# Optimization experiments

Measured on AMD Instinct MI355X. Metric: run time of the kernel, lower is better.

The kernel has to match this reference:

```python
import jax, jax.numpy as jnp
import numpy as np

N_USERS = 100000
N_ITEMS = 50000
N = N_USERS + N_ITEMS
EMBED_DIM = 64
N_LAYERS = 3
NNZ = 4800000


def setup_inputs() -> dict:
    key = jax.random.key(0)
    k1, k2, k3, k4, k5 = jax.random.split(key, 5)
    user_emb = jax.random.normal(k1, (N_USERS, EMBED_DIM), dtype=jnp.float32)
    item_emb = jax.random.normal(k2, (N_ITEMS, EMBED_DIM), dtype=jnp.float32)
    adj_row = jax.random.randint(k3, (NNZ,), 0, N, dtype=jnp.int32)
    adj_col = jax.random.randint(k4, (NNZ,), 0, N, dtype=jnp.int32)
    # normalized adjacency values (positive, small) like D^-1/2 A D^-1/2
    adj_vals = jax.random.uniform(k5, (NNZ,), dtype=jnp.float32) * 0.05
    return {"user_emb": user_emb, "item_emb": item_emb,
            "adj_row": adj_row, "adj_col": adj_col, "adj_vals": adj_vals}


def _spmm(vals, row, col, x):
    # sparse (N,N) @ dense (N,d) via gather + segment_sum
    return jax.ops.segment_sum(vals[:, None] * x[col], row, num_segments=N)


def reference(user_emb, item_emb, adj_row, adj_col, adj_vals):
    all_emb = jnp.concatenate([user_emb, item_emb], axis=0)  # (N, d)
    acc = all_emb  # running sum of layer outputs (fused mean)
    cur = all_emb
    for _ in range(N_LAYERS):
        cur = _spmm(adj_vals, adj_row, adj_col, cur)
        acc = acc + cur
    final_emb = acc / jnp.float32(N_LAYERS + 1)
    return final_emb[:N_USERS], final_emb[N_USERS:]
```

## Files before the change

kernel.cpp:

```cpp
#include <hip/hip_runtime.h>

#define N_USERS 100000
#define N_ITEMS 50000
#define N_TOTAL 150000
#define DIM 64
#define NNZ_C 4800000
#define NELEM (N_TOTAL * DIM)
#define NELEM4 (NELEM / 4)

#define RPB 74
#define NB 2048
#define NBLK 512
#define CHUNK (NNZ_C / NBLK)
#define CAP 4096

typedef unsigned short ush;

__device__ __forceinline__ float bf2f(ush u) {
    return __uint_as_float(((unsigned)u) << 16);
}
__device__ __forceinline__ ush f2bf(float f) {
    unsigned u = __float_as_uint(f);
    return (ush)((u + 0x7fffu + ((u >> 16) & 1u)) >> 16);
}

__global__ __launch_bounds__(256) void init_kernel(
    const float4* __restrict__ user, const float4* __restrict__ item,
    ushort4* __restrict__ A16) {
    int i = blockIdx.x * 256 + threadIdx.x;
    if (i >= NELEM4) return;
    const int u4 = N_USERS * DIM / 4;
    float4 v = (i < u4) ? user[i] : item[i - u4];
    ushort4 b;
    b.x = f2bf(v.x); b.y = f2bf(v.y); b.z = f2bf(v.z); b.w = f2bf(v.w);
    A16[i] = b;
}

__global__ __launch_bounds__(1024) void p1_hist(
    const int* __restrict__ row, int* __restrict__ histmat) {
    __shared__ int h[NB];
    int t = threadIdx.x, b = blockIdx.x;
    for (int j = t; j < NB; j += 1024) h[j] = 0;
    __syncthreads();
    int kbeg = b * CHUNK, kend = kbeg + CHUNK;
    for (int k = kbeg + t; k < kend; k += 1024) {
        unsigned r = (unsigned)row[k];
        atomicAdd(&h[r / RPB], 1);
    }
    __syncthreads();
    for (int j = t; j < NB; j += 1024) histmat[b * NB + j] = h[j];
}

__global__ __launch_bounds__(256) void p2a_colscan(
    const int* __restrict__ histmat, int* __restrict__ basemat,
    int* __restrict__ T) {
    int j = blockIdx.x * 256 + threadIdx.x;
    int run = 0;
    for (int b = 0; b < NBLK; b++) {
        basemat[b * NB + j] = run;
        run += histmat[b * NB + j];
    }
    T[j] = run;
}

__global__ __launch_bounds__(1024) void p2b_scan(
    const int* __restrict__ T, int* __restrict__ bucketbase,
    int* __restrict__ rowptr) {
    __shared__ int s[1024];
    int t = threadIdx.x;
    int v0 = T[2 * t], v1 = T[2 * t + 1];
    int pair = v0 + v1;
    s[t] = pair;
    __syncthreads();
    for (int off = 1; off < 1024; off <<= 1) {
        int w = (t >= off) ? s[t - off] : 0;
        __syncthreads();
        s[t] += w;
        __syncthreads();
    }
    int excl = s[t] - pair;
    bucketbase[2 * t] = excl;
    bucketbase[2 * t + 1] = excl + v0;
    if (t == 1023) { bucketbase[NB] = s[t]; rowptr[N_TOTAL] = NNZ_C; }
}

__global__ __launch_bounds__(1024) void p3_scatter(
    const int* __restrict__ row, const int* __restrict__ col,
    const float* __restrict__ vals, const int* __restrict__ histmat,
    const int* __restrict__ basemat, const int* __restrict__ bucketbase,
    uint2* __restrict__ entries) {
    __shared__ int s[1024];
    __shared__ int wp[NB];
    __shared__ int gbase[NB];
    __shared__ uint2 sorted[CHUNK];
    __shared__ int dest[CHUNK];
    int t = threadIdx.x, b = blockIdx.x;

    int c0 = histmat[b * NB + 2 * t];
    int c1 = histmat[b * NB + 2 * t + 1];
    int pair = c0 + c1;
    s[t] = pair;
    __syncthreads();
    for (int off = 1; off < 1024; off <<= 1) {
        int w = (t >= off) ? s[t - off] : 0;
        __syncthreads();
        s[t] += w;
        __syncthreads();
    }
    int excl = s[t] - pair;
    wp[2 * t] = excl;
    wp[2 * t + 1] = excl + c0;
    gbase[2 * t]     = bucketbase[2 * t]     + basemat[b * NB + 2 * t]     - excl;
    gbase[2 * t + 1] = bucketbase[2 * t + 1] + basemat[b * NB + 2 * t + 1] - (excl + c0);
    __syncthreads();

    int kbeg = b * CHUNK, kend = kbeg + CHUNK;
    for (int k = kbeg + t; k < kend; k += 1024) {
        unsigned r = (unsigned)row[k];
        unsigned j = r / RPB;
        unsigned rl = r - j * RPB;
        int pos = atomicAdd(&wp[j], 1);
        sorted[pos] = make_uint2((rl << 18) | (unsigned)col[k],
                                 __float_as_uint(vals[k]));
        dest[pos] = gbase[j] + pos;
    }
    __syncthreads();
    for (int i = t; i < CHUNK; i += 1024)
        entries[dest[i]] = sorted[i];
}

__global__ __launch_bounds__(512) void p4_sort(
    const int* __restrict__ bucketbase, uint2* __restrict__ entries,
    int* __restrict__ rowptr) {
    __shared__ uint2 stage[CAP];
    __shared__ int cnt[128], scanb[128], wp[128];
    int t = threadIdx.x, b = blockIdx.x;
    int base = bucketbase[b];
    int n = bucketbase[b + 1] - base;
    if (n > CAP) n = CAP;
    if (t < 128) cnt[t] = 0;
    __syncthreads();
    for (int i = t; i < n; i += 512) {
        uint2 e = entries[base + i];
        stage[i] = e;
        atomicAdd(&cnt[e.x >> 18], 1);
    }
    __syncthreads();
    if (t < 128) scanb[t] = cnt[t];
    __syncthreads();
    for (int off = 1; off < 128; off <<= 1) {
        int w = 0;
        if (t < 128 && t >= off) w = scanb[t - off];
        __syncthreads();
        if (t < 128) scanb[t] += w;
        __syncthreads();
    }
    if (t < RPB) {
        int excl = scanb[t] - cnt[t];
        wp[t] = excl;
        int rg = b * RPB + t;
        if (rg < N_TOTAL) rowptr[rg] = base + excl;
    }
    __syncthreads();
    for (int i = t; i < n; i += 512) {
        uint2 e = stage[i];
        unsigned rl = e.x >> 18;
        int pos = atomicAdd(&wp[rl], 1);
        ((int2*)entries)[base + pos] =
            make_int2((int)(e.x & 0x3FFFFu), (int)e.y);
    }
}

__global__ __launch_bounds__(256) void spmm_csr_kernel(
    const int* __restrict__ rowptr, const int2* __restrict__ csr,
    const ushort4* __restrict__ x4, ushort4* __restrict__ y4) {
    int gid = blockIdx.x * 256 + threadIdx.x;
    int lane = threadIdx.x & 63;
    int group = lane >> 4;
    int chunk = lane & 15;
    int r = (gid >> 6) * 4 + group;
    if (r >= N_TOTAL) return;
    int start = rowptr[r], end = rowptr[r + 1];
    float4 acc = make_float4(0.f, 0.f, 0.f, 0.f);
    for (int j0 = start; j0 < end; j0 += 16) {
        int j = j0 + chunk;
        int2 pair = make_int2(0, 0);
        if (j < end) pair = csr[j];
        int cnt = min(16, end - j0);
        #pragma unroll 4
        for (int t = 0; t < cnt; t++) {
            int src = group * 16 + t;
            int cc = __shfl(pair.x, src);
            float vv = __int_as_float(__shfl(pair.y, src));
            ushort4 xv = x4[cc * 16 + chunk];
            acc.x += vv * bf2f(xv.x);
            acc.y += vv * bf2f(xv.y);
            acc.z += vv * bf2f(xv.z);
            acc.w += vv * bf2f(xv.w);
        }
    }
    int o = r * 16 + chunk;
    ushort4 yb;
    yb.x = f2bf(acc.x); yb.y = f2bf(acc.y);
    yb.z = f2bf(acc.z); yb.w = f2bf(acc.w);
    y4[o] = yb;
}

__global__ __launch_bounds__(256) void spmm_merge_kernel(
    const int* __restrict__ rowptr, const int2* __restrict__ csr,
    const ushort4* __restrict__ x4 , const ushort4* __restrict__ e0,
    const ushort4* __restrict__ e1, float4* __restrict__ out) {
    int gid = blockIdx.x * 256 + threadIdx.x;
    int lane = threadIdx.x & 63;
    int group = lane >> 4;
    int chunk = lane & 15;
    int r = (gid >> 6) * 4 + group;
    if (r >= N_TOTAL) return;
    int start = rowptr[r], end = rowptr[r + 1];
    float4 acc = make_float4(0.f, 0.f, 0.f, 0.f);
    for (int j0 = start; j0 < end; j0 += 16) {
        int j = j0 + chunk;
        int2 pair = make_int2(0, 0);
        if (j < end) pair = csr[j];
        int cnt = min(16, end - j0);
        #pragma unroll 4
        for (int t = 0; t < cnt; t++) {
            int src = group * 16 + t;
            int cc = __shfl(pair.x, src);
            float vv = __int_as_float(__shfl(pair.y, src));
            ushort4 xv = x4[cc * 16 + chunk];
            acc.x += vv * bf2f(xv.x);
            acc.y += vv * bf2f(xv.y);
            acc.z += vv * bf2f(xv.z);
            acc.w += vv * bf2f(xv.w);
        }
    }
    int o = r * 16 + chunk;
    ushort4 a = e0[o], b = e1[o], c = x4[o];
    float4 oo;
    oo.x = (bf2f(a.x) + bf2f(b.x) + bf2f(c.x) + acc.x) * 0.25f;
    oo.y = (bf2f(a.y) + bf2f(b.y) + bf2f(c.y) + acc.y) * 0.25f;
    oo.z = (bf2f(a.z) + bf2f(b.z) + bf2f(c.z) + acc.z) * 0.25f;
    oo.w = (bf2f(a.w) + bf2f(b.w) + bf2f(c.w) + acc.w) * 0.25f;
    out[o] = oo;
}

extern "C" void kernel_launch(void* const* d_in, const int* in_sizes, int n_in,
                              void* d_out, int out_size, void* d_ws, size_t ws_size,
                              hipStream_t stream) {
    const float* user_emb = (const float*)d_in[0];
    const float* item_emb = (const float*)d_in[1];
    const int*   adj_row  = (const int*)d_in[2];
    const int*   adj_col  = (const int*)d_in[3];
    const float* adj_vals = (const float*)d_in[4];
    float* out = (float*)d_out;

    ush*   A          = (ush*)d_ws;
    ush*   B          = A + NELEM;
    ush*   C          = B + NELEM;
    uint2* entries    = (uint2*)(C + NELEM);
    int*   histmat    = (int*)(entries + NNZ_C);
    int*   basemat    = histmat + NBLK * NB;
    int*   T          = basemat + NBLK * NB;
    int*   bucketbase = T + NB;
    int*   rowptr     = bucketbase + NB + 1;

    const int eltBlocks  = (NELEM4 + 255) / 256;
    const int spmmBlocks = N_TOTAL / 16;

    init_kernel<<<eltBlocks, 256, 0, stream>>>(
        (const float4*)user_emb, (const float4*)item_emb, (ushort4*)A);
    p1_hist<<<NBLK, 1024, 0, stream>>>(adj_row, histmat);
    p2a_colscan<<<NB / 256, 256, 0, stream>>>(histmat, basemat, T);
    p2b_scan<<<1, 1024, 0, stream>>>(T, bucketbase, rowptr);
    p3_scatter<<<NBLK, 1024, 0, stream>>>(adj_row, adj_col, adj_vals,
                                          histmat, basemat, bucketbase, entries);
    p4_sort<<<NB, 512, 0, stream>>>(bucketbase, entries, rowptr);

    spmm_csr_kernel<<<spmmBlocks, 256, 0, stream>>>(rowptr, (const int2*)entries,
        (const ushort4*)A, (ushort4*)B);
    spmm_csr_kernel<<<spmmBlocks, 256, 0, stream>>>(rowptr, (const int2*)entries,
        (const ushort4*)B, (ushort4*)C);
    spmm_merge_kernel<<<spmmBlocks, 256, 0, stream>>>(rowptr, (const int2*)entries,
        (const ushort4*)C, (const ushort4*)A, (const ushort4*)B, (float4*)out);
}
```

Baseline: 539.5 us.

## Replace column-scan kernel with atomic bucket totals and atomic cursor allocation

Removes the p2a_colscan kernel, a serial walk over 512 blocks that produced a per-block base matrix. Bucket totals are now accumulated with global atomics in the histogram kernel, and each scatter block reserves its slice of a bucket with an atomicAdd on a padded cursor array. This drops one launch and the base-matrix traffic. The cost is a memset, global atomic contention on padded counters, and block order within a bucket that is no longer deterministic, which p4_sort must tolerate.

```diff
diff --git a/kernel.cpp b/kernel.cpp
--- a/kernel.cpp
+++ b/kernel.cpp
@@ -13,6 +13,7 @@
 #define NBLK 512
 #define CHUNK (NNZ_C / NBLK)
 #define CAP 4096
+#define CPAD 16
 
 typedef unsigned short ush;
 
@@ -37,7 +38,8 @@
 }
 
 __global__ __launch_bounds__(1024) void p1_hist(
-    const int* __restrict__ row, int* __restrict__ histmat) {
+    const int* __restrict__ row, int* __restrict__ histmat,
+    int* __restrict__ T) {
     __shared__ int h[NB];
     int t = threadIdx.x, b = blockIdx.x;
     for (int j = t; j < NB; j += 1024) h[j] = 0;
@@ -48,27 +50,19 @@
         atomicAdd(&h[r / RPB], 1);
     }
     __syncthreads();
-    for (int j = t; j < NB; j += 1024) histmat[b * NB + j] = h[j];
-}
-
-__global__ __launch_bounds__(256) void p2a_colscan(
-    const int* __restrict__ histmat, int* __restrict__ basemat,
-    int* __restrict__ T) {
-    int j = blockIdx.x * 256 + threadIdx.x;
-    int run = 0;
-    for (int b = 0; b < NBLK; b++) {
-        basemat[b * NB + j] = run;
-        run += histmat[b * NB + j];
-    }
-    T[j] = run;
+    for (int j = t; j < NB; j += 1024) {
+        int c = h[j];
+        histmat[b * NB + j] = c;
+        if (c) atomicAdd(&T[j * CPAD], c);
+    }
 }
 
 __global__ __launch_bounds__(1024) void p2b_scan(
     const int* __restrict__ T, int* __restrict__ bucketbase,
-    int* __restrict__ rowptr) {
+    int* __restrict__ cursor, int* __restrict__ rowptr) {
     __shared__ int s[1024];
     int t = threadIdx.x;
-    int v0 = T[2 * t], v1 = T[2 * t + 1];
+    int v0 = T[(2 * t) * CPAD], v1 = T[(2 * t + 1) * CPAD];
     int pair = v0 + v1;
     s[t] = pair;
     __syncthreads();
@@ -81,14 +75,15 @@
     int excl = s[t] - pair;
     bucketbase[2 * t] = excl;
     bucketbase[2 * t + 1] = excl + v0;
+    cursor[(2 * t) * CPAD] = excl;
+    cursor[(2 * t + 1) * CPAD] = excl + v0;
     if (t == 1023) { bucketbase[NB] = s[t]; rowptr[N_TOTAL] = NNZ_C; }
 }
 
 __global__ __launch_bounds__(1024) void p3_scatter(
     const int* __restrict__ row, const int* __restrict__ col,
     const float* __restrict__ vals, const int* __restrict__ histmat,
-    const int* __restrict__ basemat, const int* __restrict__ bucketbase,
-    uint2* __restrict__ entries) {
+    int* __restrict__ cursor, uint2* __restrict__ entries) {
     __shared__ int s[1024];
     __shared__ int wp[NB];
     __shared__ int gbase[NB];
@@ -110,8 +105,10 @@
     int excl = s[t] - pair;
     wp[2 * t] = excl;
     wp[2 * t + 1] = excl + c0;
-    gbase[2 * t]     = bucketbase[2 * t]     + basemat[b * NB + 2 * t]     - excl;
-    gbase[2 * t + 1] = bucketbase[2 * t + 1] + basemat[b * NB + 2 * t + 1] - (excl + c0);
+    int g0 = c0 ? atomicAdd(&cursor[(2 * t) * CPAD], c0) : 0;
+    int g1 = c1 ? atomicAdd(&cursor[(2 * t + 1) * CPAD], c1) : 0;
+    gbase[2 * t]     = g0 - excl;
+    gbase[2 * t + 1] = g1 - (excl + c0);
     __syncthreads();
 
     int kbeg = b * CHUNK, kend = kbeg + CHUNK;
@@ -260,21 +257,22 @@
     ush*   C          = B + NELEM;
     uint2* entries    = (uint2*)(C + NELEM);
     int*   histmat    = (int*)(entries + NNZ_C);
-    int*   basemat    = histmat + NBLK * NB;
-    int*   T          = basemat + NBLK * NB;
-    int*   bucketbase = T + NB;
+    int*   T          = histmat + NBLK * NB;
+    int*   cursor     = T + NB * CPAD;
+    int*   bucketbase = cursor + NB * CPAD;
     int*   rowptr     = bucketbase + NB + 1;
 
     const int eltBlocks  = (NELEM4 + 255) / 256;
     const int spmmBlocks = N_TOTAL / 16;
 
+    hipMemsetAsync(T, 0, NB * CPAD * sizeof(int), stream);
+
     init_kernel<<<eltBlocks, 256, 0, stream>>>(
         (const float4*)user_emb, (const float4*)item_emb, (ushort4*)A);
-    p1_hist<<<NBLK, 1024, 0, stream>>>(adj_row, histmat);
-    p2a_colscan<<<NB / 256, 256, 0, stream>>>(histmat, basemat, T);
-    p2b_scan<<<1, 1024, 0, stream>>>(T, bucketbase, rowptr);
+    p1_hist<<<NBLK, 1024, 0, stream>>>(adj_row, histmat, T);
+    p2b_scan<<<1, 1024, 0, stream>>>(T, bucketbase, cursor, rowptr);
     p3_scatter<<<NBLK, 1024, 0, stream>>>(adj_row, adj_col, adj_vals,
-                                          histmat, basemat, bucketbase, entries);
+                                          histmat, cursor, entries);
     p4_sort<<<NB, 512, 0, stream>>>(bucketbase, entries, rowptr);
 
     spmm_csr_kernel<<<spmmBlocks, 256, 0, stream>>>(rowptr, (const int2*)entries,
```

New measurement: 600.1 us. 11.2% more time.

## Parallelize column scan of block histograms with tiled three-pass scan

Applied to the files above, without the earlier changes.

Replaces the serial per-column exclusive scan over 512 block histograms, which ran on only 8 blocks of 256 threads, with a three-pass tiled scan: per-tile sums, a scan over 32 tile sums, then per-tile expansion. The aim is to spread the sequential dependency chain across many more blocks and shorten the latency of this phase. The cost is two extra kernel launches and an extra read of the histogram matrix plus small tile buffers in workspace.

```diff
diff --git a/kernel.cpp b/kernel.cpp
--- a/kernel.cpp
+++ b/kernel.cpp
@@ -13,6 +13,8 @@
 #define NBLK 512
 #define CHUNK (NNZ_C / NBLK)
 #define CAP 4096
+#define TILES 32
+#define TB (NBLK / TILES)
 
 typedef unsigned short ush;
 
@@ -51,16 +53,42 @@
     for (int j = t; j < NB; j += 1024) histmat[b * NB + j] = h[j];
 }
 
-__global__ __launch_bounds__(256) void p2a_colscan(
-    const int* __restrict__ histmat, int* __restrict__ basemat,
+__global__ __launch_bounds__(256) void p2a1_tilesum(
+    const int* __restrict__ histmat, int* __restrict__ tilesum) {
+    int j = blockIdx.x * 256 + threadIdx.x;
+    int tile = blockIdx.y;
+    int b0 = tile * TB;
+    int s = 0;
+    #pragma unroll
+    for (int i = 0; i < TB; i++) s += histmat[(b0 + i) * NB + j];
+    tilesum[tile * NB + j] = s;
+}
+
+__global__ __launch_bounds__(256) void p2a2_tilescan(
+    const int* __restrict__ tilesum, int* __restrict__ tilebase,
     int* __restrict__ T) {
     int j = blockIdx.x * 256 + threadIdx.x;
     int run = 0;
-    for (int b = 0; b < NBLK; b++) {
-        basemat[b * NB + j] = run;
-        run += histmat[b * NB + j];
+    #pragma unroll
+    for (int t = 0; t < TILES; t++) {
+        tilebase[t * NB + j] = run;
+        run += tilesum[t * NB + j];
     }
     T[j] = run;
+}
+
+__global__ __launch_bounds__(256) void p2a3_expand(
+    const int* __restrict__ histmat, const int* __restrict__ tilebase,
+    int* __restrict__ basemat) {
+    int j = blockIdx.x * 256 + threadIdx.x;
+    int tile = blockIdx.y;
+    int b0 = tile * TB;
+    int run = tilebase[tile * NB + j];
+    #pragma unroll
+    for (int i = 0; i < TB; i++) {
+        basemat[(b0 + i) * NB + j] = run;
+        run += histmat[(b0 + i) * NB + j];
+    }
 }
 
 __global__ __launch_bounds__(1024) void p2b_scan(
@@ -261,7 +289,9 @@
     uint2* entries    = (uint2*)(C + NELEM);
     int*   histmat    = (int*)(entries + NNZ_C);
     int*   basemat    = histmat + NBLK * NB;
-    int*   T          = basemat + NBLK * NB;
+    int*   tilesum    = basemat + NBLK * NB;
+    int*   tilebase   = tilesum + TILES * NB;
+    int*   T          = tilebase + TILES * NB;
     int*   bucketbase = T + NB;
     int*   rowptr     = bucketbase + NB + 1;
 
@@ -271,7 +301,10 @@
     init_kernel<<<eltBlocks, 256, 0, stream>>>(
         (const float4*)user_emb, (const float4*)item_emb, (ushort4*)A);
     p1_hist<<<NBLK, 1024, 0, stream>>>(adj_row, histmat);
-    p2a_colscan<<<NB / 256, 256, 0, stream>>>(histmat, basemat, T);
+    p2a1_tilesum<<<dim3(NB / 256, TILES), 256, 0, stream>>>(histmat, tilesum);
+    p2a2_tilescan<<<NB / 256, 256, 0, stream>>>(tilesum, tilebase, T);
+    p2a3_expand<<<dim3(NB / 256, TILES), 256, 0, stream>>>(histmat, tilebase,
+                                                           basemat);
     p2b_scan<<<1, 1024, 0, stream>>>(T, bucketbase, rowptr);
     p3_scatter<<<NBLK, 1024, 0, stream>>>(adj_row, adj_col, adj_vals,
                                           histmat, basemat, bucketbase, entries);
```

Result: faster. 516.2 us (-4.3%).
